# Kernel optimization log

Hardware: AMD Instinct MI355X
Metric: run time of the kernel (lower is better)

The kernel has to match this reference:

```python
import jax, jax.numpy as jnp
import numpy as np

DIM = 1024
DEPTH = 8
HEADS = 16
DIM_HEAD = 64
INNER = HEADS * DIM_HEAD  # 1024
NQ = 64
EMB = 768
OUT = 1024
FF_INNER = 4 * DIM
B, N1 = 32, 257
EPS = 1e-5


def layer_norm(x, g, b):
    m = jnp.mean(x, axis=-1, keepdims=True)
    v = jnp.mean(jnp.square(x - m), axis=-1, keepdims=True)
    return (x - m) * jax.lax.rsqrt(v + EPS) * g + b


def split_heads(t):
    # (b, l, inner) -> (b, h, l, dh)
    b, l, _ = t.shape
    return t.reshape(b, l, HEADS, DIM_HEAD).transpose(0, 2, 1, 3)


def setup_inputs() -> dict:
    key = jax.random.key(0)
    ks = jax.random.split(key, 12)
    s = 0.02
    inp = {
        "x": jax.random.normal(ks[0], (B, N1, EMB), jnp.float32),
        "latents": jax.random.normal(ks[1], (1, NQ, DIM), jnp.float32) / np.sqrt(DIM),
        "proj_in_w": jax.random.normal(ks[2], (EMB, DIM), jnp.float32) * s,
        "proj_in_b": jnp.zeros((DIM,), jnp.float32),
        "ln1_g": jnp.ones((DEPTH, DIM), jnp.float32),
        "ln1_b": jnp.zeros((DEPTH, DIM), jnp.float32),
        "ln2_g": jnp.ones((DEPTH, DIM), jnp.float32),
        "ln2_b": jnp.zeros((DEPTH, DIM), jnp.float32),
        "Wq": jax.random.normal(ks[3], (DEPTH, DIM, INNER), jnp.float32) * s,
        "Wkv": jax.random.normal(ks[4], (DEPTH, DIM, 2 * INNER), jnp.float32) * s,
        "Wo": jax.random.normal(ks[5], (DEPTH, INNER, DIM), jnp.float32) * s,
        "ff_ln_g": jnp.ones((DEPTH, DIM), jnp.float32),
        "ff_ln_b": jnp.zeros((DEPTH, DIM), jnp.float32),
        "ff_w1": jax.random.normal(ks[6], (DEPTH, DIM, FF_INNER), jnp.float32) * s,
        "ff_w2": jax.random.normal(ks[7], (DEPTH, FF_INNER, DIM), jnp.float32) * s,
        "proj_out_w": jax.random.uniform(ks[8], (DIM, OUT), jnp.float32, -0.01, 0.01),
        "proj_out_b": jnp.zeros((OUT,), jnp.float32),
        "norm_out_g": jnp.ones((OUT,), jnp.float32),
        "norm_out_b": jnp.zeros((OUT,), jnp.float32),
    }
    return inp


def reference(x, latents, proj_in_w, proj_in_b, ln1_g, ln1_b, ln2_g, ln2_b,
              Wq, Wkv, Wo, ff_ln_g, ff_ln_b, ff_w1, ff_w2,
              proj_out_w, proj_out_b, norm_out_g, norm_out_b):
    # proj_in
    xf = x @ proj_in_w + proj_in_b              # (b, n1, dim)
    lat = jnp.broadcast_to(latents, (x.shape[0], NQ, DIM))
    scale = DIM_HEAD ** -0.25                   # 1/sqrt(sqrt(dim_head))

    for i in range(DEPTH):
        # PerceiverAttention
        xn = layer_norm(xf, ln1_g[i], ln1_b[i])
        ln_lat = layer_norm(lat, ln2_g[i], ln2_b[i])
        q = split_heads(ln_lat @ Wq[i])                       # (b,h,nq,dh)
        kv = jnp.concatenate([xn, ln_lat], axis=1) @ Wkv[i]   # (b,n1+nq,2*inner)
        k, v = jnp.split(kv, 2, axis=-1)
        k, v = split_heads(k), split_heads(v)                 # (b,h,nk,dh)
        w = jnp.einsum('bhqd,bhkd->bhqk', q * scale, k * scale)
        w = jax.nn.softmax(w.astype(jnp.float32), axis=-1).astype(q.dtype)
        o = jnp.einsum('bhqk,bhkd->bhqd', w, v)               # (b,h,nq,dh)
        o = o.transpose(0, 2, 1, 3).reshape(lat.shape[0], NQ, INNER)
        lat = o @ Wo[i] + lat
        # FeedForward: LN -> Linear -> GELU -> Linear
        h = layer_norm(lat, ff_ln_g[i], ff_ln_b[i])
        h = jax.nn.gelu(h @ ff_w1[i], approximate=False) @ ff_w2[i]
        lat = h + lat

    out = lat @ proj_out_w + proj_out_b
    return layer_norm(out, norm_out_g, norm_out_b)
```

## Files before the change

kernel.cpp:

```cpp
#include <hip/hip_runtime.h>
#include <hip/hip_bf16.h>
#include <cstdint>

typedef __hip_bfloat16 bf16;
typedef __attribute__((ext_vector_type(8))) short short8;
typedef __attribute__((ext_vector_type(4))) float f32x4;

__device__ __forceinline__ f32x4 mfma16(short8 a, short8 b, f32x4 c) {
  return __builtin_amdgcn_mfma_f32_16x16x32_bf16(a, b, c, 0, 0, 0);
}

__device__ __forceinline__ void gload16(const bf16* g, bf16* l) {
  __builtin_amdgcn_global_load_lds((const __attribute__((address_space(1))) void*)g,
                                   (__attribute__((address_space(3))) void*)l, 16, 0, 0);
}


__global__ void __launch_bounds__(256) cvt_f32_bf16(const float* __restrict__ in,
                                                    bf16* __restrict__ out, int n4) {
  int i = blockIdx.x * 256 + threadIdx.x;
  if (i < n4) {
    float4 v = *(const float4*)&in[(size_t)i * 4];
    bf16 o[4] = {__float2bfloat16(v.x), __float2bfloat16(v.y),
                 __float2bfloat16(v.z), __float2bfloat16(v.w)};
    *(uint2*)&out[(size_t)i * 4] = *(uint2*)o;
  }
}


__device__ __forceinline__ void trans_tile64(float (*t)[65], const float* __restrict__ src,
                                             bf16* __restrict__ dst, int K, int N,
                                             int bx, int by) {
  int n0 = bx * 64, k0 = by * 64;
  int tx = threadIdx.x & 15, ty = threadIdx.x >> 4;
#pragma unroll
  for (int j = 0; j < 64; j += 16) {
    float4 v = *(const float4*)&src[(size_t)(k0 + ty + j) * N + n0 + tx * 4];
    t[ty + j][tx * 4 + 0] = v.x;
    t[ty + j][tx * 4 + 1] = v.y;
    t[ty + j][tx * 4 + 2] = v.z;
    t[ty + j][tx * 4 + 3] = v.w;
  }
  __syncthreads();
  int cb = tx * 4;
#pragma unroll
  for (int jj = 0; jj < 4; jj++) {
    int r = ty + jj * 16;
    bf16 o[4] = {__float2bfloat16(t[cb + 0][r]), __float2bfloat16(t[cb + 1][r]),
                 __float2bfloat16(t[cb + 2][r]), __float2bfloat16(t[cb + 3][r])};
    *(uint2*)&dst[(size_t)(n0 + r) * K + k0 + cb] = *(uint2*)o;
  }
}

__global__ void __launch_bounds__(256) transpose_cvt(const float* __restrict__ src,
                                                     bf16* __restrict__ dst,
                                                     int K, int N) {
  __shared__ float tile[64][65];
  trans_tile64(tile, src, dst, K, N, blockIdx.x, blockIdx.y);
}

__global__ void __launch_bounds__(256) transpose_all(
    const float* __restrict__ wq, const float* __restrict__ wkv,
    const float* __restrict__ wo, const float* __restrict__ w1,
    const float* __restrict__ w2, bf16* __restrict__ wq_t, bf16* __restrict__ wkv_t,
    bf16* __restrict__ wo_t, bf16* __restrict__ w1_t, bf16* __restrict__ w2_t) {
  __shared__ float tile[64][65];
  int id = blockIdx.x;
  if (id < 256) {
    trans_tile64(tile, wq, wq_t, 1024, 1024, id & 15, id >> 4);
  } else if (id < 768) {
    id -= 256;
    trans_tile64(tile, wkv, wkv_t, 1024, 2048, id & 31, id >> 5);
  } else if (id < 1024) {
    id -= 768;
    trans_tile64(tile, wo, wo_t, 1024, 1024, id & 15, id >> 4);
  } else if (id < 2048) {
    id -= 1024;
    trans_tile64(tile, w1, w1_t, 1024, 4096, id & 63, id >> 6);
  } else {
    id -= 2048;
    trans_tile64(tile, w2, w2_t, 4096, 1024, id & 15, id >> 4);
  }
}


__device__ __forceinline__ void stats4(float4 v, int tid, float& mean,
                                       float& rstd, float* red) {
  float s = v.x + v.y + v.z + v.w;
  float s2 = v.x * v.x + v.y * v.y + v.z * v.z + v.w * v.w;
#pragma unroll
  for (int o = 32; o > 0; o >>= 1) {
    s += __shfl_down(s, o);
    s2 += __shfl_down(s2, o);
  }
  int w = tid >> 6;
  if ((tid & 63) == 0) { red[w] = s; red[4 + w] = s2; }
  __syncthreads();
  s = red[0] + red[1] + red[2] + red[3];
  s2 = red[4] + red[5] + red[6] + red[7];
  mean = s * (1.f / 1024.f);
  float var = s2 * (1.f / 1024.f) - mean * mean;
  rstd = rsqrtf(var + 1e-5f);
}

__device__ __forceinline__ void pack4(bf16* dst, float a, float b, float c, float d) {
  bf16 o[4] = {__float2bfloat16(a), __float2bfloat16(b),
               __float2bfloat16(c), __float2bfloat16(d)};
  *(uint2*)dst = *(uint2*)o;
}

__global__ void __launch_bounds__(256) ln_to_bf16(const float* __restrict__ in,
                                                  const float* __restrict__ g,
                                                  const float* __restrict__ bb,
                                                  bf16* __restrict__ out) {
  __shared__ float red[8];
  int row = blockIdx.x, tid = threadIdx.x, c4 = tid * 4;
  float4 v = *(const float4*)&in[(size_t)row * 1024 + c4];
  float mean, rstd;
  stats4(v, tid, mean, rstd, red);
  float y0 = (v.x - mean) * rstd, y1 = (v.y - mean) * rstd;
  float y2 = (v.z - mean) * rstd, y3 = (v.w - mean) * rstd;
  if (g) {
    float4 gv = *(const float4*)&g[c4];
    float4 bv = *(const float4*)&bb[c4];
    y0 = y0 * gv.x + bv.x; y1 = y1 * gv.y + bv.y;
    y2 = y2 * gv.z + bv.z; y3 = y3 * gv.w + bv.w;
  }
  pack4(&out[(size_t)row * 1024 + c4], y0, y1, y2, y3);
}

template <int LM>
__global__ void __launch_bounds__(256) lncat(const bf16* __restrict__ xhat,
                                             const float* __restrict__ lin,
                                             const float* __restrict__ parts,
                                             const float* __restrict__ lat2,
                                             float* __restrict__ lat,
                                             const float* __restrict__ g1,
                                             const float* __restrict__ b1,
                                             const float* __restrict__ g2,
                                             const float* __restrict__ b2,
                                             bf16* __restrict__ cat,
                                             bf16* __restrict__ lnlat) {
  __shared__ float red[8];
  int row = blockIdx.x, tid = threadIdx.x, c4 = tid * 4;
  int bidx = row / 336, n = row - bidx * 336;
  bf16* out = cat + (size_t)row * 1024;
  const size_t MN = (size_t)2048 * 1024;
  if (n < 257) {
    const bf16* in = xhat + ((size_t)bidx * 257 + n) * 1024;
    uint2 rw = *(const uint2*)&in[c4];
    const bf16* rb = (const bf16*)&rw;
    float4 gv = *(const float4*)&g1[c4];
    float4 bv = *(const float4*)&b1[c4];
    pack4(&out[c4], __bfloat162float(rb[0]) * gv.x + bv.x,
          __bfloat162float(rb[1]) * gv.y + bv.y,
          __bfloat162float(rb[2]) * gv.z + bv.z,
          __bfloat162float(rb[3]) * gv.w + bv.w);
  } else if (n < 321) {
    int lrow = bidx * 64 + (n - 257);
    size_t idx = (size_t)lrow * 1024 + c4;
    float4 a;
    if (LM == 0) {
      a = *(const float4*)&lin[(size_t)(n - 257) * 1024 + c4];
    } else {
      float4 p0 = *(const float4*)&parts[idx];
      float4 p1 = *(const float4*)&parts[MN + idx];
      float4 p2 = *(const float4*)&parts[2 * MN + idx];
      float4 p3 = *(const float4*)&parts[3 * MN + idx];
      float4 r2 = *(const float4*)&lat2[idx];
      a.x = p0.x + p1.x + p2.x + p3.x + r2.x;
      a.y = p0.y + p1.y + p2.y + p3.y + r2.y;
      a.z = p0.z + p1.z + p2.z + p3.z + r2.z;
      a.w = p0.w + p1.w + p2.w + p3.w + r2.w;
    }
    *(float4*)&lat[idx] = a;
    float mean, rstd;
    stats4(a, tid, mean, rstd, red);
    float4 gv = *(const float4*)&g2[c4];
    float4 bv = *(const float4*)&b2[c4];
    bf16 o[4] = {__float2bfloat16((a.x - mean) * rstd * gv.x + bv.x),
                 __float2bfloat16((a.y - mean) * rstd * gv.y + bv.y),
                 __float2bfloat16((a.z - mean) * rstd * gv.z + bv.z),
                 __float2bfloat16((a.w - mean) * rstd * gv.w + bv.w)};
    *(uint2*)&out[c4] = *(uint2*)o;
    *(uint2*)&lnlat[idx] = *(uint2*)o;
  } else {
    uint2 z = {0, 0};
    *(uint2*)&out[c4] = z;
  }
}


enum { MB_BIAS = 1, MB_RESID = 2, MB_GELU = 4, MB_BF16 = 8 };

template <int MODE>
__device__ __forceinline__ void gemm_tile(
    const bf16* __restrict__ A, const bf16* __restrict__ Bt, void* __restrict__ Cout,
    const float* __restrict__ bias, const float* __restrict__ resid,
    int M, int N, int K, int m0, int n0, int kBeg, int kEnd, size_t planeOff,
    bf16* sA, bf16* sB) {
  int tid = threadIdx.x;
  int wave = tid >> 6, lane = tid & 63;
  int quad = lane >> 4, l16 = lane & 15;
  int wm = (wave >> 1) * 64, wn = (wave & 1) * 64;

  int srow = wave * 16 + (lane >> 2);
  int scol = (lane & 3) * 8;
  const bf16* gA0 = A + (size_t)min(m0 + srow, M - 1) * K + scol;
  const bf16* gA1 = A + (size_t)min(m0 + 64 + srow, M - 1) * K + scol;
  const bf16* gB0 = Bt + (size_t)(n0 + srow) * K + scol;
  const bf16* gB1 = Bt + (size_t)(n0 + 64 + srow) * K + scol;
  bf16* lA0 = &sA[(wave * 16) * 32];
  bf16* lA1 = &sA[(64 + wave * 16) * 32];
  bf16* lB0 = &sB[(wave * 16) * 32];
  bf16* lB1 = &sB[(64 + wave * 16) * 32];

  f32x4 acc[4][4] = {};

  for (int k0 = kBeg; k0 < kEnd; k0 += 32) {
    gload16(gA0 + k0, lA0);
    gload16(gA1 + k0, lA1);
    gload16(gB0 + k0, lB0);
    gload16(gB1 + k0, lB1);
    __syncthreads();
    short8 af[4], bfv[4];
#pragma unroll
    for (int i = 0; i < 4; i++)
      af[i] = *(const short8*)&sA[(wm + i * 16 + l16) * 32 + quad * 8];
#pragma unroll
    for (int j = 0; j < 4; j++)
      bfv[j] = *(const short8*)&sB[(wn + j * 16 + l16) * 32 + quad * 8];
#pragma unroll
    for (int i = 0; i < 4; i++)
#pragma unroll
      for (int j = 0; j < 4; j++)
        acc[i][j] = mfma16(af[i], bfv[j], acc[i][j]);
    __syncthreads();
  }

  float* cf = (float*)Cout + planeOff;
#pragma unroll
  for (int i = 0; i < 4; i++) {
    int grb = m0 + wm + i * 16 + quad * 4;
#pragma unroll
    for (int j = 0; j < 4; j++) {
      int gc = n0 + wn + j * 16 + l16;
      float bv = (MODE & MB_BIAS) ? bias[gc] : 0.f;
#pragma unroll
      for (int r = 0; r < 4; r++) {
        int gr = grb + r;
        if (gr < M) {
          float vv = acc[i][j][r] + bv;
          if (MODE & MB_GELU) vv = 0.5f * vv * (1.f + erff(vv * 0.70710678118654752f));
          if (MODE & MB_RESID) vv += resid[(size_t)gr * N + gc];
          if (MODE & MB_BF16) ((bf16*)Cout)[(size_t)gr * N + gc] = __float2bfloat16(vv);
          else cf[(size_t)gr * N + gc] = vv;
        }
      }
    }
  }
}

template <int MODE>
__global__ void __launch_bounds__(256, 2) gemm_bt(
    const bf16* __restrict__ A, const bf16* __restrict__ Bt,
    void* __restrict__ Cout, const float* __restrict__ bias,
    const float* __restrict__ resid, int M, int N, int K) {
  __shared__ bf16 sA[128 * 32];
  __shared__ bf16 sB[128 * 32];
  int kPer = K / gridDim.z;
  gemm_tile<MODE>(A, Bt, Cout, bias, resid, M, N, K,
                  blockIdx.y * 128, blockIdx.x * 128,
                  blockIdx.z * kPer, (blockIdx.z + 1) * kPer,
                  (size_t)blockIdx.z * ((size_t)M * N), sA, sB);
}

__global__ void __launch_bounds__(256, 2) gemm_qkv(
    const bf16* __restrict__ catb, const bf16* __restrict__ wkv,
    bf16* __restrict__ kvbuf, const bf16* __restrict__ lnlat,
    const bf16* __restrict__ wq, bf16* __restrict__ qbuf) {
  __shared__ bf16 sA[128 * 32];
  __shared__ bf16 sB[128 * 32];
  int by = blockIdx.y, bx = blockIdx.x;
  if (by < 84) {
    gemm_tile<MB_BF16>(catb, wkv, kvbuf, nullptr, nullptr, 10752, 2048, 1024,
                       by * 128, bx * 128, 0, 1024, 0, sA, sB);
  } else {
    int t = (by - 84) * 16 + bx;
    gemm_tile<MB_BF16>(lnlat, wq, qbuf, nullptr, nullptr, 2048, 1024, 1024,
                       (t >> 3) * 128, (t & 7) * 128, 0, 1024, 0, sA, sB);
  }
}


enum { RD_BIAS = 1, RD_RESID = 2, RD_BF16 = 4 };

template <int MODE>
__global__ void __launch_bounds__(256) reduce_k(const float* __restrict__ parts, int S,
                                                int MN, int N,
                                                const float* __restrict__ bias,
                                                const float* __restrict__ resid,
                                                void* __restrict__ out) {
  int i4 = (blockIdx.x * 256 + threadIdx.x) * 4;
  if (i4 >= MN) return;
  float4 a = *(const float4*)&parts[i4];
#pragma unroll 4
  for (int s = 1; s < S; s++) {
    float4 b = *(const float4*)&parts[(size_t)s * MN + i4];
    a.x += b.x; a.y += b.y; a.z += b.z; a.w += b.w;
  }
  if (MODE & RD_BIAS) {
    float4 b = *(const float4*)&bias[i4 & (N - 1)];
    a.x += b.x; a.y += b.y; a.z += b.z; a.w += b.w;
  }
  if (MODE & RD_RESID) {
    float4 b = *(const float4*)&resid[i4];
    a.x += b.x; a.y += b.y; a.z += b.z; a.w += b.w;
  }
  if (MODE & RD_BF16) {
    bf16 o[4] = {__float2bfloat16(a.x), __float2bfloat16(a.y),
                 __float2bfloat16(a.z), __float2bfloat16(a.w)};
    *(uint2*)&((bf16*)out)[i4] = *(uint2*)o;
  } else {
    *(float4*)&((float*)out)[i4] = a;
  }
}

__global__ void __launch_bounds__(256) reduce_ln_resid(
    const float* __restrict__ parts, const float* __restrict__ resid,
    const float* __restrict__ g, const float* __restrict__ bb,
    float* __restrict__ lat2, bf16* __restrict__ lnff) {
  __shared__ float red[8];
  int row = blockIdx.x, tid = threadIdx.x, c4 = tid * 4;
  const size_t MN = (size_t)2048 * 1024;
  size_t idx = (size_t)row * 1024 + c4;
  float4 p0 = *(const float4*)&parts[idx];
  float4 p1 = *(const float4*)&parts[MN + idx];
  float4 p2 = *(const float4*)&parts[2 * MN + idx];
  float4 p3 = *(const float4*)&parts[3 * MN + idx];
  float4 r2 = *(const float4*)&resid[idx];
  float4 a;
  a.x = p0.x + p1.x + p2.x + p3.x + r2.x;
  a.y = p0.y + p1.y + p2.y + p3.y + r2.y;
  a.z = p0.z + p1.z + p2.z + p3.z + r2.z;
  a.w = p0.w + p1.w + p2.w + p3.w + r2.w;
  *(float4*)&lat2[idx] = a;
  float mean, rstd;
  stats4(a, tid, mean, rstd, red);
  float4 gv = *(const float4*)&g[c4];
  float4 bv = *(const float4*)&bb[c4];
  pack4(&lnff[idx], (a.x - mean) * rstd * gv.x + bv.x,
        (a.y - mean) * rstd * gv.y + bv.y,
        (a.z - mean) * rstd * gv.z + bv.z,
        (a.w - mean) * rstd * gv.w + bv.w);
}

__global__ void __launch_bounds__(256) reduce_bias_ln(
    const float* __restrict__ parts, const float* __restrict__ bias,
    const float* __restrict__ g, const float* __restrict__ bb,
    float* __restrict__ out) {
  __shared__ float red[8];
  int row = blockIdx.x, tid = threadIdx.x, c4 = tid * 4;
  const size_t MN = (size_t)2048 * 1024;
  size_t idx = (size_t)row * 1024 + c4;
  float4 p0 = *(const float4*)&parts[idx];
  float4 p1 = *(const float4*)&parts[MN + idx];
  float4 p2 = *(const float4*)&parts[2 * MN + idx];
  float4 p3 = *(const float4*)&parts[3 * MN + idx];
  float4 bv = *(const float4*)&bias[c4];
  float4 a;
  a.x = p0.x + p1.x + p2.x + p3.x + bv.x;
  a.y = p0.y + p1.y + p2.y + p3.y + bv.y;
  a.z = p0.z + p1.z + p2.z + p3.z + bv.z;
  a.w = p0.w + p1.w + p2.w + p3.w + bv.w;
  float mean, rstd;
  stats4(a, tid, mean, rstd, red);
  float4 gv = *(const float4*)&g[c4];
  float4 b2 = *(const float4*)&bb[c4];
  float4 o;
  o.x = (a.x - mean) * rstd * gv.x + b2.x;
  o.y = (a.y - mean) * rstd * gv.y + b2.y;
  o.z = (a.z - mean) * rstd * gv.z + b2.z;
  o.w = (a.w - mean) * rstd * gv.w + b2.w;
  *(float4*)&out[idx] = o;
}


__device__ __forceinline__ int swz64(int row, int cb) {
  return (row << 7) + (cb ^ ((row & 7) << 4) ^ (((row >> 3) & 3) << 5));
}

__global__ void __launch_bounds__(256, 2) attn(const bf16* __restrict__ qb,
                                               const bf16* __restrict__ kvb,
                                               bf16* __restrict__ ob) {
  __shared__ bf16 sQ[64 * 64];
  __shared__ bf16 sKV[64 * 64];
  __shared__ bf16 sP[64 * 376];
  __shared__ float sRed[256];
  char* cQ = (char*)sQ;
  char* cKV = (char*)sKV;

  int h = blockIdx.x, b = blockIdx.y;
  int tid = threadIdx.x, wave = tid >> 6, lane = tid & 63;
  int quad = lane >> 4, l16 = lane & 15;

  const bf16* qg = qb + (size_t)b * 64 * 1024 + h * 64;
  const bf16* kg = kvb + (size_t)b * 336 * 2048 + h * 64;
  const bf16* vg = kg + 1024;

  {
    int r = tid >> 3, cb = (tid & 7) * 16;
    *(uint4*)(cQ + swz64(r, cb)) =
        *(const uint4*)((const char*)qg + (size_t)r * 2048 + cb);
    *(uint4*)(cQ + swz64(r + 32, cb)) =
        *(const uint4*)((const char*)qg + (size_t)(r + 32) * 2048 + cb);
  }

  f32x4 accS[6][4] = {};

  for (int g = 0; g < 6; g++) {
    __syncthreads();
    {
      int r = tid >> 3, cb = (tid & 7) * 16;
      int gr = g * 64 + r;
      if (gr < 336)
        *(uint4*)(cKV + swz64(r, cb)) =
            *(const uint4*)((const char*)kg + (size_t)gr * 4096 + cb);
      gr += 32;
      if (gr < 336)
        *(uint4*)(cKV + swz64(r + 32, cb)) =
            *(const uint4*)((const char*)kg + (size_t)gr * 4096 + cb);
    }
    __syncthreads();
    if (g * 4 + wave < 21) {
#pragma unroll
      for (int ks = 0; ks < 2; ks++) {
        short8 bfr = *(const short8*)(cKV + swz64(wave * 16 + l16, ks * 64 + quad * 16));
#pragma unroll
        for (int i = 0; i < 4; i++) {
          short8 afr = *(const short8*)(cQ + swz64(i * 16 + l16, ks * 64 + quad * 16));
          accS[g][i] = mfma16(afr, bfr, accS[g][i]);
        }
      }
    }
  }

  float rmax[4][4], rsum[4][4];
#pragma unroll
  for (int i = 0; i < 4; i++)
#pragma unroll
    for (int r = 0; r < 4; r++) { rmax[i][r] = -1e30f; rsum[i][r] = 0.f; }

#pragma unroll
  for (int g = 0; g < 6; g++) {
    int col = (g * 4 + wave) * 16 + l16;
    bool valid = col < 321;
#pragma unroll
    for (int i = 0; i < 4; i++)
#pragma unroll
      for (int r = 0; r < 4; r++) {
        float v = accS[g][i][r] * 0.125f;
        accS[g][i][r] = v;
        if (valid) rmax[i][r] = fmaxf(rmax[i][r], v);
      }
  }
#pragma unroll
  for (int off = 1; off < 16; off <<= 1)
#pragma unroll
    for (int i = 0; i < 4; i++)
#pragma unroll
      for (int r = 0; r < 4; r++)
        rmax[i][r] = fmaxf(rmax[i][r], __shfl_xor(rmax[i][r], off));
  if (l16 == 0) {
#pragma unroll
    for (int i = 0; i < 4; i++)
#pragma unroll
      for (int r = 0; r < 4; r++)
        sRed[wave * 64 + i * 16 + quad * 4 + r] = rmax[i][r];
  }
  __syncthreads();
#pragma unroll
  for (int i = 0; i < 4; i++)
#pragma unroll
    for (int r = 0; r < 4; r++) {
      int row = i * 16 + quad * 4 + r;
      rmax[i][r] = fmaxf(fmaxf(sRed[row], sRed[64 + row]),
                         fmaxf(sRed[128 + row], sRed[192 + row]));
    }
  __syncthreads();

#pragma unroll
  for (int g = 0; g < 6; g++) {
    int col = (g * 4 + wave) * 16 + l16;
    bool valid = col < 321;
#pragma unroll
    for (int i = 0; i < 4; i++)
#pragma unroll
      for (int r = 0; r < 4; r++) {
        float pv = valid ? __expf(accS[g][i][r] - rmax[i][r]) : 0.f;
        rsum[i][r] += pv;
        if (col < 352) sP[(i * 16 + quad * 4 + r) * 376 + col] = __float2bfloat16(pv);
      }
  }
#pragma unroll
  for (int off = 1; off < 16; off <<= 1)
#pragma unroll
    for (int i = 0; i < 4; i++)
#pragma unroll
      for (int r = 0; r < 4; r++)
        rsum[i][r] += __shfl_xor(rsum[i][r], off);
  if (l16 == 0) {
#pragma unroll
    for (int i = 0; i < 4; i++)
#pragma unroll
      for (int r = 0; r < 4; r++)
        sRed[wave * 64 + i * 16 + quad * 4 + r] = rsum[i][r];
  }
  __syncthreads();
#pragma unroll
  for (int i = 0; i < 4; i++)
#pragma unroll
    for (int r = 0; r < 4; r++) {
      int row = i * 16 + quad * 4 + r;
      rsum[i][r] = sRed[row] + sRed[64 + row] + sRed[128 + row] + sRed[192 + row];
    }

  f32x4 accO[4] = {};
  for (int cch = 0; cch < 6; cch++) {
    __syncthreads();
    {
      int r = tid >> 3, cb = (tid & 7) * 16;
      int gr = cch * 64 + r;
      if (gr < 336)
        *(uint4*)(cKV + swz64(r, cb)) =
            *(const uint4*)((const char*)vg + (size_t)gr * 4096 + cb);
      gr += 32;
      if (gr < 336)
        *(uint4*)(cKV + swz64(r + 32, cb)) =
            *(const uint4*)((const char*)vg + (size_t)gr * 4096 + cb);
    }
    __syncthreads();
    int nks = (cch == 5) ? 1 : 2;
    for (int ks = 0; ks < nks; ks++) {
      short8 bv;
      int cb = (wave * 16 + l16) * 2;
#pragma unroll
      for (int jj = 0; jj < 8; jj++)
        bv[jj] = *(const short*)(cKV + swz64(ks * 32 + quad * 8 + jj, cb));
#pragma unroll
      for (int i = 0; i < 4; i++) {
        short8 ap = *(const short8*)&sP[(i * 16 + l16) * 376 + cch * 64 + ks * 32 + quad * 8];
        accO[i] = mfma16(ap, bv, accO[i]);
      }
    }
  }

#pragma unroll
  for (int i = 0; i < 4; i++)
#pragma unroll
    for (int r = 0; r < 4; r++) {
      int row = i * 16 + quad * 4 + r;
      ob[(size_t)(b * 64 + row) * 1024 + h * 64 + wave * 16 + l16] =
          __float2bfloat16(accO[i][r] / rsum[i][r]);
    }
}


extern "C" void kernel_launch(void* const* d_in, const int* in_sizes, int n_in,
                              void* d_out, int out_size, void* d_ws, size_t ws_size,
                              hipStream_t stream) {
  (void)in_sizes; (void)n_in; (void)out_size; (void)ws_size;
  const float* x    = (const float*)d_in[0];
  const float* lin  = (const float*)d_in[1];
  const float* piw  = (const float*)d_in[2];
  const float* pib  = (const float*)d_in[3];
  const float* ln1g = (const float*)d_in[4];
  const float* ln1b = (const float*)d_in[5];
  const float* ln2g = (const float*)d_in[6];
  const float* ln2b = (const float*)d_in[7];
  const float* Wq   = (const float*)d_in[8];
  const float* Wkv  = (const float*)d_in[9];
  const float* Wo   = (const float*)d_in[10];
  const float* ffg  = (const float*)d_in[11];
  const float* ffb  = (const float*)d_in[12];
  const float* W1   = (const float*)d_in[13];
  const float* W2   = (const float*)d_in[14];
  const float* poW  = (const float*)d_in[15];
  const float* pob  = (const float*)d_in[16];
  const float* nog  = (const float*)d_in[17];
  const float* nob  = (const float*)d_in[18];

  char* p = (char*)d_ws;
  auto alloc = [&](size_t bytes) -> char* {
    char* q = p; p += (bytes + 255) & ~(size_t)255; return q;
  };
  bf16* pin_t  = (bf16*)alloc((size_t)1024 * 768 * 2);
  bf16* pout_t = (bf16*)alloc((size_t)1024 * 1024 * 2);
  bf16* wq_t   = (bf16*)alloc((size_t)1024 * 1024 * 2);
  bf16* wkv_t  = (bf16*)alloc((size_t)2048 * 1024 * 2);
  bf16* wo_t   = (bf16*)alloc((size_t)1024 * 1024 * 2);
  bf16* w1_t   = (bf16*)alloc((size_t)4096 * 1024 * 2);
  bf16* w2_t   = (bf16*)alloc((size_t)1024 * 4096 * 2);
  bf16* x_bf   = (bf16*)alloc((size_t)8224 * 768 * 2);
  float* xf    = (float*)alloc((size_t)8224 * 1024 * 4);
  bf16* xhat   = (bf16*)alloc((size_t)8224 * 1024 * 2);
  bf16* cat    = (bf16*)alloc((size_t)10752 * 1024 * 2);
  bf16* lnlat  = (bf16*)alloc((size_t)2048 * 1024 * 2);
  bf16* qbuf   = (bf16*)alloc((size_t)2048 * 1024 * 2);
  bf16* kvbuf  = (bf16*)alloc((size_t)10752 * 2048 * 2);
  bf16* obuf   = (bf16*)alloc((size_t)2048 * 1024 * 2);
  float* lat   = (float*)alloc((size_t)2048 * 1024 * 4);
  float* lat2  = (float*)alloc((size_t)2048 * 1024 * 4);
  bf16* lnff   = (bf16*)alloc((size_t)2048 * 1024 * 2);
  bf16* h1     = (bf16*)alloc((size_t)2048 * 4096 * 2);

  const int MN = 2048 * 1024;

  cvt_f32_bf16<<<(6316032 / 4 + 255) / 256, 256, 0, stream>>>(x, x_bf, 6316032 / 4);
  transpose_cvt<<<dim3(16, 12), 256, 0, stream>>>(piw, pin_t, 768, 1024);
  transpose_cvt<<<dim3(16, 16), 256, 0, stream>>>(poW, pout_t, 1024, 1024);
  gemm_bt<MB_BIAS><<<dim3(8, 65), 256, 0, stream>>>(x_bf, pin_t, xf, pib, nullptr,
                                                    8224, 1024, 768);
  ln_to_bf16<<<8224, 256, 0, stream>>>(xf, nullptr, nullptr, xhat);

  for (int i = 0; i < 8; i++) {
    transpose_all<<<3072, 256, 0, stream>>>(
        Wq + (size_t)i * 1048576, Wkv + (size_t)i * 2097152, Wo + (size_t)i * 1048576,
        W1 + (size_t)i * 4194304, W2 + (size_t)i * 4194304,
        wq_t, wkv_t, wo_t, w1_t, w2_t);
    if (i == 0)
      lncat<0><<<10752, 256, 0, stream>>>(xhat, lin, nullptr, nullptr, lat,
                                          ln1g + i * 1024, ln1b + i * 1024,
                                          ln2g + i * 1024, ln2b + i * 1024, cat, lnlat);
    else
      lncat<1><<<10752, 256, 0, stream>>>(xhat, nullptr, xf, lat2, lat,
                                          ln1g + i * 1024, ln1b + i * 1024,
                                          ln2g + i * 1024, ln2b + i * 1024, cat, lnlat);
    gemm_qkv<<<dim3(16, 92), 256, 0, stream>>>(cat, wkv_t, kvbuf, lnlat, wq_t, qbuf);
    attn<<<dim3(16, 32), 256, 0, stream>>>(qbuf, kvbuf, obuf);
    gemm_bt<0><<<dim3(8, 16, 4), 256, 0, stream>>>(obuf, wo_t, xf, nullptr, nullptr,
                                                   2048, 1024, 1024);
    reduce_ln_resid<<<2048, 256, 0, stream>>>(xf, lat, ffg + i * 1024, ffb + i * 1024,
                                              lat2, lnff);
    gemm_bt<MB_GELU | MB_BF16><<<dim3(32, 16), 256, 0, stream>>>(lnff, w1_t, h1, nullptr,
                                                                 nullptr, 2048, 4096, 1024);
    gemm_bt<0><<<dim3(8, 16, 4), 256, 0, stream>>>(h1, w2_t, xf, nullptr, nullptr,
                                                   2048, 1024, 4096);
    if (i == 7)
      reduce_k<RD_RESID | RD_BF16><<<MN / 1024, 256, 0, stream>>>(
          xf, 4, MN, 1024, nullptr, lat2, lnff);
  }

  gemm_bt<0><<<dim3(8, 16, 4), 256, 0, stream>>>(lnff, pout_t, xf, nullptr, nullptr,
                                                 2048, 1024, 1024);
  reduce_bias_ln<<<2048, 256, 0, stream>>>(xf, pob, nog, nob, (float*)d_out);
}
```

Before: 1.991 ms.

## Batch all-layer weight transposes into one launch and restructure attention loads

All eight layers' weights are transposed and converted in a single up-front launch over a 2D grid, and each layer's GEMMs index into per-layer slices of larger workspace buffers. This removes seven launches and lets the transpose run with much more parallelism, at the cost of more workspace memory. Separately, the attention kernel reads K fragments directly from global memory instead of staging them through shared memory, dropping two barriers per tile. V chunks are also prefetched into registers one iteration ahead to hide global latency.

Result: slower. 2.122 ms (+6.6%).

```diff
diff --git a/kernel.cpp b/kernel.cpp
--- a/kernel.cpp
+++ b/kernel.cpp
@@ -66,20 +66,22 @@
     bf16* __restrict__ wo_t, bf16* __restrict__ w1_t, bf16* __restrict__ w2_t) {
   __shared__ float tile[64][65];
   int id = blockIdx.x;
+  size_t L = blockIdx.y;
+  size_t oq = L * 1048576, okv = L * 2097152, o1 = L * 4194304;
   if (id < 256) {
-    trans_tile64(tile, wq, wq_t, 1024, 1024, id & 15, id >> 4);
+    trans_tile64(tile, wq + oq, wq_t + oq, 1024, 1024, id & 15, id >> 4);
   } else if (id < 768) {
     id -= 256;
-    trans_tile64(tile, wkv, wkv_t, 1024, 2048, id & 31, id >> 5);
+    trans_tile64(tile, wkv + okv, wkv_t + okv, 1024, 2048, id & 31, id >> 5);
   } else if (id < 1024) {
     id -= 768;
-    trans_tile64(tile, wo, wo_t, 1024, 1024, id & 15, id >> 4);
+    trans_tile64(tile, wo + oq, wo_t + oq, 1024, 1024, id & 15, id >> 4);
   } else if (id < 2048) {
     id -= 1024;
-    trans_tile64(tile, w1, w1_t, 1024, 4096, id & 63, id >> 6);
+    trans_tile64(tile, w1 + o1, w1_t + o1, 1024, 4096, id & 63, id >> 6);
   } else {
     id -= 2048;
-    trans_tile64(tile, w2, w2_t, 4096, 1024, id & 15, id >> 4);
+    trans_tile64(tile, w2 + o1, w2_t + o1, 4096, 1024, id & 15, id >> 4);
   }
 }
 
@@ -394,11 +396,11 @@
                                                const bf16* __restrict__ kvb,
                                                bf16* __restrict__ ob) {
   __shared__ bf16 sQ[64 * 64];
-  __shared__ bf16 sKV[64 * 64];
+  __shared__ bf16 sV[64 * 64];
   __shared__ bf16 sP[64 * 376];
   __shared__ float sRed[256];
   char* cQ = (char*)sQ;
-  char* cKV = (char*)sKV;
+  char* cV = (char*)sV;
 
   int h = blockIdx.x, b = blockIdx.y;
   int tid = threadIdx.x, wave = tid >> 6, lane = tid & 63;
@@ -408,38 +410,26 @@
   const bf16* kg = kvb + (size_t)b * 336 * 2048 + h * 64;
   const bf16* vg = kg + 1024;
 
-  {
-    int r = tid >> 3, cb = (tid & 7) * 16;
-    *(uint4*)(cQ + swz64(r, cb)) =
-        *(const uint4*)((const char*)qg + (size_t)r * 2048 + cb);
-    *(uint4*)(cQ + swz64(r + 32, cb)) =
-        *(const uint4*)((const char*)qg + (size_t)(r + 32) * 2048 + cb);
-  }
+  int r = tid >> 3, cb8 = (tid & 7) * 16;
+  *(uint4*)(cQ + swz64(r, cb8)) =
+      *(const uint4*)((const char*)qg + (size_t)r * 2048 + cb8);
+  *(uint4*)(cQ + swz64(r + 32, cb8)) =
+      *(const uint4*)((const char*)qg + (size_t)(r + 32) * 2048 + cb8);
+  __syncthreads();
 
   f32x4 accS[6][4] = {};
-
-  for (int g = 0; g < 6; g++) {
-    __syncthreads();
-    {
-      int r = tid >> 3, cb = (tid & 7) * 16;
-      int gr = g * 64 + r;
-      if (gr < 336)
-        *(uint4*)(cKV + swz64(r, cb)) =
-            *(const uint4*)((const char*)kg + (size_t)gr * 4096 + cb);
-      gr += 32;
-      if (gr < 336)
-        *(uint4*)(cKV + swz64(r + 32, cb)) =
-            *(const uint4*)((const char*)kg + (size_t)gr * 4096 + cb);
-    }
-    __syncthreads();
-    if (g * 4 + wave < 21) {
+#pragma unroll
+  for (int s = 0; s < 6; s++) {
+    int t = s * 4 + wave;
+    if (t < 21) {
+      const char* krow = (const char*)kg + (size_t)(t * 16 + l16) * 4096;
 #pragma unroll
       for (int ks = 0; ks < 2; ks++) {
-        short8 bfr = *(const short8*)(cKV + swz64(wave * 16 + l16, ks * 64 + quad * 16));
+        short8 bfr = *(const short8*)(krow + ks * 64 + quad * 16);
 #pragma unroll
         for (int i = 0; i < 4; i++) {
           short8 afr = *(const short8*)(cQ + swz64(i * 16 + l16, ks * 64 + quad * 16));
-          accS[g][i] = mfma16(afr, bfr, accS[g][i]);
+          accS[s][i] = mfma16(afr, bfr, accS[s][i]);
         }
       }
     }
@@ -449,19 +439,19 @@
 #pragma unroll
   for (int i = 0; i < 4; i++)
 #pragma unroll
-    for (int r = 0; r < 4; r++) { rmax[i][r] = -1e30f; rsum[i][r] = 0.f; }
-
-#pragma unroll
-  for (int g = 0; g < 6; g++) {
-    int col = (g * 4 + wave) * 16 + l16;
+    for (int rr = 0; rr < 4; rr++) { rmax[i][rr] = -1e30f; rsum[i][rr] = 0.f; }
+
+#pragma unroll
+  for (int s = 0; s < 6; s++) {
+    int col = (s * 4 + wave) * 16 + l16;
     bool valid = col < 321;
 #pragma unroll
     for (int i = 0; i < 4; i++)
 #pragma unroll
-      for (int r = 0; r < 4; r++) {
-        float v = accS[g][i][r] * 0.125f;
-        accS[g][i][r] = v;
-        if (valid) rmax[i][r] = fmaxf(rmax[i][r], v);
+      for (int rr = 0; rr < 4; rr++) {
+        float v = accS[s][i][rr] * 0.125f;
+        accS[s][i][rr] = v;
+        if (valid) rmax[i][rr] = fmaxf(rmax[i][rr], v);
       }
   }
 #pragma unroll
@@ -469,37 +459,37 @@
 #pragma unroll
     for (int i = 0; i < 4; i++)
 #pragma unroll
-      for (int r = 0; r < 4; r++)
-        rmax[i][r] = fmaxf(rmax[i][r], __shfl_xor(rmax[i][r], off));
+      for (int rr = 0; rr < 4; rr++)
+        rmax[i][rr] = fmaxf(rmax[i][rr], __shfl_xor(rmax[i][rr], off));
   if (l16 == 0) {
 #pragma unroll
     for (int i = 0; i < 4; i++)
 #pragma unroll
-      for (int r = 0; r < 4; r++)
-        sRed[wave * 64 + i * 16 + quad * 4 + r] = rmax[i][r];
+      for (int rr = 0; rr < 4; rr++)
+        sRed[wave * 64 + i * 16 + quad * 4 + rr] = rmax[i][rr];
   }
   __syncthreads();
 #pragma unroll
   for (int i = 0; i < 4; i++)
 #pragma unroll
-    for (int r = 0; r < 4; r++) {
-      int row = i * 16 + quad * 4 + r;
-      rmax[i][r] = fmaxf(fmaxf(sRed[row], sRed[64 + row]),
-                         fmaxf(sRed[128 + row], sRed[192 + row]));
+    for (int rr = 0; rr < 4; rr++) {
+      int row = i * 16 + quad * 4 + rr;
+      rmax[i][rr] = fmaxf(fmaxf(sRed[row], sRed[64 + row]),
+                          fmaxf(sRed[128 + row], sRed[192 + row]));
     }
   __syncthreads();
 
 #pragma unroll
-  for (int g = 0; g < 6; g++) {
-    int col = (g * 4 + wave) * 16 + l16;
+  for (int s = 0; s < 6; s++) {
+    int col = (s * 4 + wave) * 16 + l16;
     bool valid = col < 321;
 #pragma unroll
     for (int i = 0; i < 4; i++)
 #pragma unroll
-      for (int r = 0; r < 4; r++) {
-        float pv = valid ? __expf(accS[g][i][r] - rmax[i][r]) : 0.f;
-        rsum[i][r] += pv;
-        if (col < 352) sP[(i * 16 + quad * 4 + r) * 376 + col] = __float2bfloat16(pv);
+      for (int rr = 0; rr < 4; rr++) {
+        float pv = valid ? __expf(accS[s][i][rr] - rmax[i][rr]) : 0.f;
+        rsum[i][rr] += pv;
+        if (col < 352) sP[(i * 16 + quad * 4 + rr) * 376 + col] = __float2bfloat16(pv);
       }
   }
 #pragma unroll
@@ -507,37 +497,41 @@
 #pragma unroll
     for (int i = 0; i < 4; i++)
 #pragma unroll
-      for (int r = 0; r < 4; r++)
-        rsum[i][r] += __shfl_xor(rsum[i][r], off);
+      for (int rr = 0; rr < 4; rr++)
+        rsum[i][rr] += __shfl_xor(rsum[i][rr], off);
   if (l16 == 0) {
 #pragma unroll
     for (int i = 0; i < 4; i++)
 #pragma unroll
-      for (int r = 0; r < 4; r++)
-        sRed[wave * 64 + i * 16 + quad * 4 + r] = rsum[i][r];
+      for (int rr = 0; rr < 4; rr++)
+        sRed[wave * 64 + i * 16 + quad * 4 + rr] = rsum[i][rr];
   }
   __syncthreads();
 #pragma unroll
   for (int i = 0; i < 4; i++)
 #pragma unroll
-    for (int r = 0; r < 4; r++) {
-      int row = i * 16 + quad * 4 + r;
-      rsum[i][r] = sRed[row] + sRed[64 + row] + sRed[128 + row] + sRed[192 + row];
+    for (int rr = 0; rr < 4; rr++) {
+      int row = i * 16 + quad * 4 + rr;
+      rsum[i][rr] = sRed[row] + sRed[64 + row] + sRed[128 + row] + sRed[192 + row];
     }
 
   f32x4 accO[4] = {};
+  uint4 v0, v1;
+  {
+    v0 = *(const uint4*)((const char*)vg + (size_t)r * 4096 + cb8);
+    v1 = *(const uint4*)((const char*)vg + (size_t)(r + 32) * 4096 + cb8);
+  }
   for (int cch = 0; cch < 6; cch++) {
     __syncthreads();
     {
-      int r = tid >> 3, cb = (tid & 7) * 16;
-      int gr = cch * 64 + r;
-      if (gr < 336)
-        *(uint4*)(cKV + swz64(r, cb)) =
-            *(const uint4*)((const char*)vg + (size_t)gr * 4096 + cb);
-      gr += 32;
-      if (gr < 336)
-        *(uint4*)(cKV + swz64(r + 32, cb)) =
-            *(const uint4*)((const char*)vg + (size_t)gr * 4096 + cb);
+      int g0 = cch * 64 + r, g1 = g0 + 32;
+      if (g0 < 336) *(uint4*)(cV + swz64(r, cb8)) = v0;
+      if (g1 < 336) *(uint4*)(cV + swz64(r + 32, cb8)) = v1;
+    }
+    if (cch < 5) {
+      int g0 = (cch + 1) * 64 + r, g1 = g0 + 32;
+      if (g0 < 336) v0 = *(const uint4*)((const char*)vg + (size_t)g0 * 4096 + cb8);
+      if (g1 < 336) v1 = *(const uint4*)((const char*)vg + (size_t)g1 * 4096 + cb8);
     }
     __syncthreads();
     int nks = (cch == 5) ? 1 : 2;
@@ -546,7 +540,7 @@
       int cb = (wave * 16 + l16) * 2;
 #pragma unroll
       for (int jj = 0; jj < 8; jj++)
-        bv[jj] = *(const short*)(cKV + swz64(ks * 32 + quad * 8 + jj, cb));
+        bv[jj] = *(const short*)(cV + swz64(ks * 32 + quad * 8 + jj, cb));
 #pragma unroll
       for (int i = 0; i < 4; i++) {
         short8 ap = *(const short8*)&sP[(i * 16 + l16) * 376 + cch * 64 + ks * 32 + quad * 8];
@@ -558,10 +552,10 @@
 #pragma unroll
   for (int i = 0; i < 4; i++)
 #pragma unroll
-    for (int r = 0; r < 4; r++) {
-      int row = i * 16 + quad * 4 + r;
+    for (int rr = 0; rr < 4; rr++) {
+      int row = i * 16 + quad * 4 + rr;
       ob[(size_t)(b * 64 + row) * 1024 + h * 64 + wave * 16 + l16] =
-          __float2bfloat16(accO[i][r] / rsum[i][r]);
+          __float2bfloat16(accO[i][rr] / rsum[i][rr]);
     }
 }
 
@@ -596,11 +590,11 @@
   };
   bf16* pin_t  = (bf16*)alloc((size_t)1024 * 768 * 2);
   bf16* pout_t = (bf16*)alloc((size_t)1024 * 1024 * 2);
-  bf16* wq_t   = (bf16*)alloc((size_t)1024 * 1024 * 2);
-  bf16* wkv_t  = (bf16*)alloc((size_t)2048 * 1024 * 2);
-  bf16* wo_t   = (bf16*)alloc((size_t)1024 * 1024 * 2);
-  bf16* w1_t   = (bf16*)alloc((size_t)4096 * 1024 * 2);
-  bf16* w2_t   = (bf16*)alloc((size_t)1024 * 4096 * 2);
+  bf16* wq_t   = (bf16*)alloc((size_t)8 * 1048576 * 2);
+  bf16* wkv_t  = (bf16*)alloc((size_t)8 * 2097152 * 2);
+  bf16* wo_t   = (bf16*)alloc((size_t)8 * 1048576 * 2);
+  bf16* w1_t   = (bf16*)alloc((size_t)8 * 4194304 * 2);
+  bf16* w2_t   = (bf16*)alloc((size_t)8 * 4194304 * 2);
   bf16* x_bf   = (bf16*)alloc((size_t)8224 * 768 * 2);
   float* xf    = (float*)alloc((size_t)8224 * 1024 * 4);
   bf16* xhat   = (bf16*)alloc((size_t)8224 * 1024 * 2);
@@ -619,15 +613,13 @@
   cvt_f32_bf16<<<(6316032 / 4 + 255) / 256, 256, 0, stream>>>(x, x_bf, 6316032 / 4);
   transpose_cvt<<<dim3(16, 12), 256, 0, stream>>>(piw, pin_t, 768, 1024);
   transpose_cvt<<<dim3(16, 16), 256, 0, stream>>>(poW, pout_t, 1024, 1024);
+  transpose_all<<<dim3(3072, 8), 256, 0, stream>>>(Wq, Wkv, Wo, W1, W2,
+                                                   wq_t, wkv_t, wo_t, w1_t, w2_t);
   gemm_bt<MB_BIAS><<<dim3(8, 65), 256, 0, stream>>>(x_bf, pin_t, xf, pib, nullptr,
                                                     8224, 1024, 768);
   ln_to_bf16<<<8224, 256, 0, stream>>>(xf, nullptr, nullptr, xhat);
 
   for (int i = 0; i < 8; i++) {
-    transpose_all<<<3072, 256, 0, stream>>>(
-        Wq + (size_t)i * 1048576, Wkv + (size_t)i * 2097152, Wo + (size_t)i * 1048576,
-        W1 + (size_t)i * 4194304, W2 + (size_t)i * 4194304,
-        wq_t, wkv_t, wo_t, w1_t, w2_t);
     if (i == 0)
       lncat<0><<<10752, 256, 0, stream>>>(xhat, lin, nullptr, nullptr, lat,
                                           ln1g + i * 1024, ln1b + i * 1024,
@@ -636,16 +628,17 @@
       lncat<1><<<10752, 256, 0, stream>>>(xhat, nullptr, xf, lat2, lat,
                                           ln1g + i * 1024, ln1b + i * 1024,
                                           ln2g + i * 1024, ln2b + i * 1024, cat, lnlat);
-    gemm_qkv<<<dim3(16, 92), 256, 0, stream>>>(cat, wkv_t, kvbuf, lnlat, wq_t, qbuf);
+    gemm_qkv<<<dim3(16, 92), 256, 0, stream>>>(cat, wkv_t + (size_t)i * 2097152, kvbuf,
+                                               lnlat, wq_t + (size_t)i * 1048576, qbuf);
     attn<<<dim3(16, 32), 256, 0, stream>>>(qbuf, kvbuf, obuf);
-    gemm_bt<0><<<dim3(8, 16, 4), 256, 0, stream>>>(obuf, wo_t, xf, nullptr, nullptr,
-                                                   2048, 1024, 1024);
+    gemm_bt<0><<<dim3(8, 16, 4), 256, 0, stream>>>(obuf, wo_t + (size_t)i * 1048576, xf,
+                                                   nullptr, nullptr, 2048, 1024, 1024);
     reduce_ln_resid<<<2048, 256, 0, stream>>>(xf, lat, ffg + i * 1024, ffb + i * 1024,
                                               lat2, lnff);
-    gemm_bt<MB_GELU | MB_BF16><<<dim3(32, 16), 256, 0, stream>>>(lnff, w1_t, h1, nullptr,
-                                                                 nullptr, 2048, 4096, 1024);
-    gemm_bt<0><<<dim3(8, 16, 4), 256, 0, stream>>>(h1, w2_t, xf, nullptr, nullptr,
-                                                   2048, 1024, 4096);
+    gemm_bt<MB_GELU | MB_BF16><<<dim3(32, 16), 256, 0, stream>>>(
+        lnff, w1_t + (size_t)i * 4194304, h1, nullptr, nullptr, 2048, 4096, 1024);
+    gemm_bt<0><<<dim3(8, 16, 4), 256, 0, stream>>>(h1, w2_t + (size_t)i * 4194304, xf,
+                                                   nullptr, nullptr, 2048, 1024, 4096);
     if (i == 7)
       reduce_k<RD_RESID | RD_BF16><<<MN / 1024, 256, 0, stream>>>(
           xf, 4, MN, 1024, nullptr, lat2, lnff);
```
